# Optimization experiments

Measured on AMD Instinct MI355X. Metric: run time of the kernel, lower is better.

The kernel has to match this reference:

```python
import jax, jax.numpy as jnp
import numpy as np

N = 100000
E = 1600000
D_IN = 64
D_H = 64
D_OUT = 10
EPS_BN = 1e-5
EPS_NORM = 1e-12


def setup_inputs() -> dict:
    key = jax.random.key(0)
    ks = jax.random.split(key, 16)
    x = jax.random.normal(ks[0], (N, D_IN), dtype=jnp.float32)
    edge_index = jax.random.randint(ks[1], (2, E), 0, N, dtype=jnp.int64)
    def lin(k, fo, fi):
        s = 1.0 / np.sqrt(fi)
        return jax.random.uniform(k, (fo, fi), jnp.float32, -s, s)
    return {
        "x": x, "edge_index": edge_index,
        "Wl1": lin(ks[2], D_H, D_IN), "Wr1": lin(ks[3], D_H, D_IN), "b1": jnp.zeros((D_H,), jnp.float32),
        "g1": jnp.ones((D_H,), jnp.float32), "be1": jnp.zeros((D_H,), jnp.float32),
        "Wl2": lin(ks[4], D_H, D_H), "Wr2": lin(ks[5], D_H, D_H), "b2": jnp.zeros((D_H,), jnp.float32),
        "g2": jnp.ones((D_H,), jnp.float32), "be2": jnp.zeros((D_H,), jnp.float32),
        "Wl3": lin(ks[6], D_OUT, D_H), "Wr3": lin(ks[7], D_OUT, D_H), "b3": jnp.zeros((D_OUT,), jnp.float32),
    }


def _sage_conv(x, src, dst, Wl, Wr, b, normalize):
    # mean aggregation over incoming edges (messages flow src -> dst)
    agg = jax.ops.segment_sum(x[src], dst, num_segments=N)
    cnt = jax.ops.segment_sum(jnp.ones((src.shape[0],), x.dtype), dst, num_segments=N)
    mean = agg / jnp.clip(cnt, 1.0)[:, None]
    out = mean @ Wl.T + x @ Wr.T + b
    if normalize:
        nrm = jnp.sqrt(jnp.sum(out * out, axis=-1, keepdims=True))
        out = out / jnp.maximum(nrm, EPS_NORM)
    return out


def _batchnorm(x, gamma, beta):
    mu = jnp.mean(x, axis=0)
    var = jnp.mean((x - mu) ** 2, axis=0)  # biased var (training mode)
    return (x - mu) * jax.lax.rsqrt(var + EPS_BN) * gamma + beta


def reference(x, edge_index, Wl1, Wr1, b1, g1, be1, Wl2, Wr2, b2, g2, be2, Wl3, Wr3, b3):
    src, dst = edge_index[0], edge_index[1]
    h = _sage_conv(x, src, dst, Wl1, Wr1, b1, True)
    h = jax.nn.relu(_batchnorm(h, g1, be1))
    h = _sage_conv(h, src, dst, Wl2, Wr2, b2, True)
    h = jax.nn.relu(_batchnorm(h, g2, be2))
    h = _sage_conv(h, src, dst, Wl3, Wr3, b3, False)
    return h
```

## Files before the change

### kernel.cpp

```cpp
#include <hip/hip_runtime.h>
#include <hip/hip_bf16.h>

#define NN 100000
#define EE 1600000
#define BSZ 512
#define NBKT 196
#define CHUNK 8192
#define NCH 196

typedef short bf16x8 __attribute__((ext_vector_type(8)));
typedef float f32x4 __attribute__((ext_vector_type(4)));

__device__ inline unsigned short bf16_of(float f) {
    __hip_bfloat16 h = __float2bfloat16(f);
    return *reinterpret_cast<unsigned short*>(&h);
}
__device__ inline unsigned pack2(float a, float b) {
    return (unsigned)bf16_of(a) | ((unsigned)bf16_of(b) << 16);
}
__device__ inline float bflo(unsigned u) { return __uint_as_float(u << 16); }
__device__ inline float bfhi(unsigned u) { return __uint_as_float(u & 0xffff0000u); }


__global__ __launch_bounds__(256)
void k_ccount(const int* __restrict__ ei, int* __restrict__ ccount) {
    __shared__ int hist[NBKT];
    int tid = threadIdx.x;
    int e0 = blockIdx.x * CHUNK;
    int e1 = e0 + CHUNK; if (e1 > EE) e1 = EE;
    for (int i = tid; i < NBKT; i += 256) hist[i] = 0;
    __syncthreads();
    for (int e = e0 + tid; e < e1; e += 256)
        atomicAdd(&hist[ei[EE + e] >> 9], 1);
    __syncthreads();
    for (int i = tid; i < NBKT; i += 256)
        if (hist[i]) atomicAdd(&ccount[i], hist[i]);
}

__global__ void k_cscan(const int* __restrict__ ccount, int* __restrict__ cbase,
                        int* __restrict__ gcur) {
    __shared__ int s[256];
    int tid = threadIdx.x;
    int v = (tid < NBKT) ? ccount[tid] : 0;
    s[tid] = v;
    __syncthreads();
    for (int off = 1; off < 256; off <<= 1) {
        int t = (tid >= off) ? s[tid - off] : 0;
        __syncthreads();
        if (tid >= off) s[tid] += t;
        __syncthreads();
    }
    if (tid < NBKT) {
        int excl = s[tid] - v;
        cbase[tid] = excl;
        gcur[tid] = excl;
    }
    if (tid == NBKT - 1) cbase[NBKT] = s[tid];
}

__global__ __launch_bounds__(256)
void k_coarse(const int* __restrict__ ei, int* __restrict__ gcur, int* __restrict__ pairs) {
    __shared__ int hist[NBKT];
    __shared__ int base[NBKT];
    __shared__ int curs[NBKT];
    int tid = threadIdx.x;
    int e0 = blockIdx.x * CHUNK;
    int e1 = e0 + CHUNK; if (e1 > EE) e1 = EE;
    for (int i = tid; i < NBKT; i += 256) hist[i] = 0;
    __syncthreads();
    for (int e = e0 + tid; e < e1; e += 256)
        atomicAdd(&hist[ei[EE + e] >> 9], 1);
    __syncthreads();
    for (int i = tid; i < NBKT; i += 256) {
        base[i] = atomicAdd(&gcur[i], hist[i]);
        curs[i] = 0;
    }
    __syncthreads();
    for (int e = e0 + tid; e < e1; e += 256) {
        int src = ei[e];
        int dst = ei[EE + e];
        int b = dst >> 9;
        int off = atomicAdd(&curs[b], 1);
        pairs[base[b] + off] = (src << 9) | (dst & 511);
    }
}

__global__ __launch_bounds__(512)
void k_fine(const int* __restrict__ cbase, const int* __restrict__ pairs,
            int* __restrict__ rs, int* __restrict__ esrc) {
    __shared__ int deg[BSZ];
    __shared__ int s[BSZ];
    int b = blockIdx.x;
    int n0 = b * BSZ;
    int nlocal = NN - n0; if (nlocal > BSZ) nlocal = BSZ;
    int tid = threadIdx.x;
    deg[tid] = 0;
    __syncthreads();
    int e0 = cbase[b], e1 = cbase[b + 1];
    for (int e = e0 + tid; e < e1; e += 512)
        atomicAdd(&deg[pairs[e] & 511], 1);
    __syncthreads();
    int v = deg[tid];
    s[tid] = v;
    __syncthreads();
    for (int off = 1; off < 512; off <<= 1) {
        int t = (tid >= off) ? s[tid - off] : 0;
        __syncthreads();
        if (tid >= off) s[tid] += t;
        __syncthreads();
    }
    int excl = s[tid] - v;
    if (tid < nlocal) rs[n0 + tid] = e0 + excl;
    if (b == NBKT - 1 && tid == 0) rs[NN] = EE;
    deg[tid] = e0 + excl;
    __syncthreads();
    for (int e = e0 + tid; e < e1; e += 512) {
        int pk = pairs[e];
        int pos = atomicAdd(&deg[pk & 511], 1);
        esrc[pos] = pk >> 9;
    }
}

__global__ void k_tobf(const float4* __restrict__ src, ushort4* __restrict__ dst) {
    int i = blockIdx.x * 256 + threadIdx.x;
    if (i >= NN * 16) return;
    float4 v = src[i];
    dst[i] = make_ushort4(bf16_of(v.x), bf16_of(v.y), bf16_of(v.z), bf16_of(v.w));
}

__global__ void k_packW(const float* __restrict__ Wl1, const float* __restrict__ Wr1,
                        const float* __restrict__ Wl2, const float* __restrict__ Wr2,
                        unsigned short* __restrict__ w1, unsigned short* __restrict__ w2) {
    int tid = threadIdx.x;
    for (int i = tid; i < 8192; i += 256) {
        int n = i >> 7, k = i & 127;
        float v1 = (k < 64) ? Wl1[n * 64 + k] : Wr1[n * 64 + (k - 64)];
        w1[i] = bf16_of(v1);
        float v2 = (k < 64) ? Wl2[n * 64 + k] : Wr2[n * 64 + (k - 64)];
        w2[i] = bf16_of(v2);
    }
}

__global__ __launch_bounds__(256, 8)
void k_aggbf(const unsigned short* __restrict__ xbf, const int* __restrict__ rs,
             const int* __restrict__ esrc, unsigned short* __restrict__ meanbf,
             const float* __restrict__ sc, const float* __restrict__ sh) {
    int gid = blockIdx.x * 256 + threadIdx.x;
    int node = gid >> 6;
    if (node >= NN) return;
    int lane = threadIdx.x & 63;
    int c = lane & 7;
    int slot = lane >> 3;
    int s0 = rs[node], s1 = rs[node + 1];
    const uint4* xb = (const uint4*)xbf;
    float a0 = 0.f, a1 = 0.f, a2 = 0.f, a3 = 0.f, a4 = 0.f, a5 = 0.f, a6 = 0.f, a7 = 0.f;
    if (sc) {
        float4 scl = ((const float4*)sc)[2 * c], sch = ((const float4*)sc)[2 * c + 1];
        float4 shl = ((const float4*)sh)[2 * c], shh = ((const float4*)sh)[2 * c + 1];
        int p = s0 + slot;
        for (; p + 8 < s1; p += 16) {
            uint4 va = xb[esrc[p] * 8 + c];
            uint4 vb = xb[esrc[p + 8] * 8 + c];
            a0 += fmaxf(fmaf(bflo(va.x), scl.x, shl.x), 0.f);
            a1 += fmaxf(fmaf(bfhi(va.x), scl.y, shl.y), 0.f);
            a2 += fmaxf(fmaf(bflo(va.y), scl.z, shl.z), 0.f);
            a3 += fmaxf(fmaf(bfhi(va.y), scl.w, shl.w), 0.f);
            a4 += fmaxf(fmaf(bflo(va.z), sch.x, shh.x), 0.f);
            a5 += fmaxf(fmaf(bfhi(va.z), sch.y, shh.y), 0.f);
            a6 += fmaxf(fmaf(bflo(va.w), sch.z, shh.z), 0.f);
            a7 += fmaxf(fmaf(bfhi(va.w), sch.w, shh.w), 0.f);
            a0 += fmaxf(fmaf(bflo(vb.x), scl.x, shl.x), 0.f);
            a1 += fmaxf(fmaf(bfhi(vb.x), scl.y, shl.y), 0.f);
            a2 += fmaxf(fmaf(bflo(vb.y), scl.z, shl.z), 0.f);
            a3 += fmaxf(fmaf(bfhi(vb.y), scl.w, shl.w), 0.f);
            a4 += fmaxf(fmaf(bflo(vb.z), sch.x, shh.x), 0.f);
            a5 += fmaxf(fmaf(bfhi(vb.z), sch.y, shh.y), 0.f);
            a6 += fmaxf(fmaf(bflo(vb.w), sch.z, shh.z), 0.f);
            a7 += fmaxf(fmaf(bfhi(vb.w), sch.w, shh.w), 0.f);
        }
        if (p < s1) {
            uint4 va = xb[esrc[p] * 8 + c];
            a0 += fmaxf(fmaf(bflo(va.x), scl.x, shl.x), 0.f);
            a1 += fmaxf(fmaf(bfhi(va.x), scl.y, shl.y), 0.f);
            a2 += fmaxf(fmaf(bflo(va.y), scl.z, shl.z), 0.f);
            a3 += fmaxf(fmaf(bfhi(va.y), scl.w, shl.w), 0.f);
            a4 += fmaxf(fmaf(bflo(va.z), sch.x, shh.x), 0.f);
            a5 += fmaxf(fmaf(bfhi(va.z), sch.y, shh.y), 0.f);
            a6 += fmaxf(fmaf(bflo(va.w), sch.z, shh.z), 0.f);
            a7 += fmaxf(fmaf(bfhi(va.w), sch.w, shh.w), 0.f);
        }
    } else {
        int p = s0 + slot;
        for (; p + 8 < s1; p += 16) {
            uint4 va = xb[esrc[p] * 8 + c];
            uint4 vb = xb[esrc[p + 8] * 8 + c];
            a0 += bflo(va.x) + bflo(vb.x); a1 += bfhi(va.x) + bfhi(vb.x);
            a2 += bflo(va.y) + bflo(vb.y); a3 += bfhi(va.y) + bfhi(vb.y);
            a4 += bflo(va.z) + bflo(vb.z); a5 += bfhi(va.z) + bfhi(vb.z);
            a6 += bflo(va.w) + bflo(vb.w); a7 += bfhi(va.w) + bfhi(vb.w);
        }
        if (p < s1) {
            uint4 va = xb[esrc[p] * 8 + c];
            a0 += bflo(va.x); a1 += bfhi(va.x);
            a2 += bflo(va.y); a3 += bfhi(va.y);
            a4 += bflo(va.z); a5 += bfhi(va.z);
            a6 += bflo(va.w); a7 += bfhi(va.w);
        }
    }
#pragma unroll
    for (int m = 8; m <= 32; m <<= 1) {
        a0 += __shfl_xor(a0, m, 64); a1 += __shfl_xor(a1, m, 64);
        a2 += __shfl_xor(a2, m, 64); a3 += __shfl_xor(a3, m, 64);
        a4 += __shfl_xor(a4, m, 64); a5 += __shfl_xor(a5, m, 64);
        a6 += __shfl_xor(a6, m, 64); a7 += __shfl_xor(a7, m, 64);
    }
    if (slot == 0) {
        int cnt = s1 - s0; if (cnt < 1) cnt = 1;
        float inv = 1.0f / (float)cnt;
        uint4 o;
        o.x = pack2(a0 * inv, a1 * inv);
        o.y = pack2(a2 * inv, a3 * inv);
        o.z = pack2(a4 * inv, a5 * inv);
        o.w = pack2(a6 * inv, a7 * inv);
        ((uint4*)meanbf)[node * 8 + c] = o;
    }
}

__global__ __launch_bounds__(256, 4)
void k_sagemfma(const unsigned short* __restrict__ meanbf,
                const unsigned short* __restrict__ a2bf,
                const unsigned short* __restrict__ Wbf,
                const float* __restrict__ bias,
                unsigned short* __restrict__ outbf,
                float* __restrict__ partials,
                const float* __restrict__ sc, const float* __restrict__ sh) {
    __shared__ float sblk[64];
    __shared__ float qblk[64];
    const int tid = threadIdx.x;
    const int base = blockIdx.x * 64;
    const int col = tid & 15;
    const int q   = (tid >> 4) & 3;
    const int w   = tid >> 6;

    if (tid < 64) { sblk[tid] = 0.f; qblk[tid] = 0.f; }

    int gn = base + w * 16 + col; if (gn > NN - 1) gn = NN - 1;
    const uint4* mb = (const uint4*)meanbf;
    const uint4* ab = (const uint4*)a2bf;
    const uint4* wb = (const uint4*)Wbf;

    uint4 fa0 = mb[gn * 8 + q];
    uint4 fa1 = mb[gn * 8 + 4 + q];
    uint4 fa2 = ab[gn * 8 + q];
    uint4 fa3 = ab[gn * 8 + 4 + q];
    if (sc) {
        float4 s0 = ((const float4*)sc)[q * 2],     s1 = ((const float4*)sc)[q * 2 + 1];
        float4 h0 = ((const float4*)sh)[q * 2],     h1 = ((const float4*)sh)[q * 2 + 1];
        float4 s2 = ((const float4*)sc)[8 + q * 2], s3 = ((const float4*)sc)[8 + q * 2 + 1];
        float4 h2 = ((const float4*)sh)[8 + q * 2], h3 = ((const float4*)sh)[8 + q * 2 + 1];
        fa2.x = pack2(fmaxf(fmaf(bflo(fa2.x), s0.x, h0.x), 0.f),
                      fmaxf(fmaf(bfhi(fa2.x), s0.y, h0.y), 0.f));
        fa2.y = pack2(fmaxf(fmaf(bflo(fa2.y), s0.z, h0.z), 0.f),
                      fmaxf(fmaf(bfhi(fa2.y), s0.w, h0.w), 0.f));
        fa2.z = pack2(fmaxf(fmaf(bflo(fa2.z), s1.x, h1.x), 0.f),
                      fmaxf(fmaf(bfhi(fa2.z), s1.y, h1.y), 0.f));
        fa2.w = pack2(fmaxf(fmaf(bflo(fa2.w), s1.z, h1.z), 0.f),
                      fmaxf(fmaf(bfhi(fa2.w), s1.w, h1.w), 0.f));
        fa3.x = pack2(fmaxf(fmaf(bflo(fa3.x), s2.x, h2.x), 0.f),
                      fmaxf(fmaf(bfhi(fa3.x), s2.y, h2.y), 0.f));
        fa3.y = pack2(fmaxf(fmaf(bflo(fa3.y), s2.z, h2.z), 0.f),
                      fmaxf(fmaf(bfhi(fa3.y), s2.w, h2.w), 0.f));
        fa3.z = pack2(fmaxf(fmaf(bflo(fa3.z), s3.x, h3.x), 0.f),
                      fmaxf(fmaf(bfhi(fa3.z), s3.y, h3.y), 0.f));
        fa3.w = pack2(fmaxf(fmaf(bflo(fa3.w), s3.z, h3.z), 0.f),
                      fmaxf(fmaf(bfhi(fa3.w), s3.w, h3.w), 0.f));
    }
    uint4 fa[4] = {fa0, fa1, fa2, fa3};

    f32x4 acc0 = {0.f, 0.f, 0.f, 0.f}, acc1 = acc0, acc2 = acc0, acc3 = acc0;
#pragma unroll
    for (int c = 0; c < 4; ++c) {
        uint4 b0 = wb[(0 * 16 + col) * 16 + c * 4 + q];
        uint4 b1 = wb[(1 * 16 + col) * 16 + c * 4 + q];
        uint4 b2 = wb[(2 * 16 + col) * 16 + c * 4 + q];
        uint4 b3 = wb[(3 * 16 + col) * 16 + c * 4 + q];
        bf16x8 a = *(const bf16x8*)&fa[c];
        acc0 = __builtin_amdgcn_mfma_f32_16x16x32_bf16(a, *(const bf16x8*)&b0, acc0, 0, 0, 0);
        acc1 = __builtin_amdgcn_mfma_f32_16x16x32_bf16(a, *(const bf16x8*)&b1, acc1, 0, 0, 0);
        acc2 = __builtin_amdgcn_mfma_f32_16x16x32_bf16(a, *(const bf16x8*)&b2, acc2, 0, 0, 0);
        acc3 = __builtin_amdgcn_mfma_f32_16x16x32_bf16(a, *(const bf16x8*)&b3, acc3, 0, 0, 0);
    }

    float bb0 = bias[col], bb1 = bias[16 + col], bb2 = bias[32 + col], bb3 = bias[48 + col];
    float sj0 = 0.f, sj1 = 0.f, sj2 = 0.f, sj3 = 0.f;
    float qj0 = 0.f, qj1 = 0.f, qj2 = 0.f, qj3 = 0.f;
#pragma unroll
    for (int r = 0; r < 4; ++r) {
        int go = base + w * 16 + q * 4 + r;
        float o0 = acc0[r] + bb0, o1 = acc1[r] + bb1;
        float o2 = acc2[r] + bb2, o3 = acc3[r] + bb3;
        float ssv = o0 * o0 + o1 * o1 + o2 * o2 + o3 * o3;
        ssv += __shfl_xor(ssv, 1, 64);
        ssv += __shfl_xor(ssv, 2, 64);
        ssv += __shfl_xor(ssv, 4, 64);
        ssv += __shfl_xor(ssv, 8, 64);
        float inv = 1.0f / fmaxf(sqrtf(ssv), 1e-12f);
        o0 *= inv; o1 *= inv; o2 *= inv; o3 *= inv;
        if (go < NN) {
            outbf[go * 64 + col]      = bf16_of(o0);
            outbf[go * 64 + 16 + col] = bf16_of(o1);
            outbf[go * 64 + 32 + col] = bf16_of(o2);
            outbf[go * 64 + 48 + col] = bf16_of(o3);
            sj0 += o0; sj1 += o1; sj2 += o2; sj3 += o3;
            qj0 += o0 * o0; qj1 += o1 * o1; qj2 += o2 * o2; qj3 += o3 * o3;
        }
    }
#pragma unroll
    for (int m = 16; m <= 32; m <<= 1) {
        sj0 += __shfl_xor(sj0, m, 64); sj1 += __shfl_xor(sj1, m, 64);
        sj2 += __shfl_xor(sj2, m, 64); sj3 += __shfl_xor(sj3, m, 64);
        qj0 += __shfl_xor(qj0, m, 64); qj1 += __shfl_xor(qj1, m, 64);
        qj2 += __shfl_xor(qj2, m, 64); qj3 += __shfl_xor(qj3, m, 64);
    }
    __syncthreads();
    if (q == 0) {
        atomicAdd(&sblk[col], sj0);      atomicAdd(&qblk[col], qj0);
        atomicAdd(&sblk[16 + col], sj1); atomicAdd(&qblk[16 + col], qj1);
        atomicAdd(&sblk[32 + col], sj2); atomicAdd(&qblk[32 + col], qj2);
        atomicAdd(&sblk[48 + col], sj3); atomicAdd(&qblk[48 + col], qj3);
    }
    __syncthreads();
    if (tid < 128)
        partials[blockIdx.x * 128 + tid] = (tid < 64) ? sblk[tid] : qblk[tid - 64];
}

__global__ __launch_bounds__(256)
void k_bnred(const float* __restrict__ partials, int nblk, float* __restrict__ red) {
    __shared__ float s[256];
    int tid = threadIdx.x;
    int idx = tid & 127, half = tid >> 7;
    float a0 = 0.f, a1 = 0.f, a2 = 0.f, a3 = 0.f;
    int r = blockIdx.x * 2 + half;
    for (; r + 192 < nblk; r += 256) {
        a0 += partials[r * 128 + idx];
        a1 += partials[(r + 64) * 128 + idx];
        a2 += partials[(r + 128) * 128 + idx];
        a3 += partials[(r + 192) * 128 + idx];
    }
    for (; r < nblk; r += 64) a0 += partials[r * 128 + idx];
    s[tid] = (a0 + a1) + (a2 + a3);
    __syncthreads();
    if (tid < 128) red[blockIdx.x * 128 + tid] = s[tid] + s[tid + 128];
}

__global__ void k_bnfin(const float* __restrict__ red,
                        const float* __restrict__ g, const float* __restrict__ be,
                        float* __restrict__ scale, float* __restrict__ shift) {
    __shared__ float s[256];
    int tid = threadIdx.x;
    int idx = tid & 127, half = tid >> 7;
    float a = 0.f;
#pragma unroll
    for (int r = half; r < 32; r += 2)
        a += red[r * 128 + idx];
    s[tid] = a;
    __syncthreads();
    if (tid < 128) s[tid] += s[tid + 128];
    __syncthreads();
    if (tid < 64) {
        float mu = s[tid] / (float)NN;
        float var = s[64 + tid] / (float)NN - mu * mu;
        var = fmaxf(var, 0.0f);
        float sc = g[tid] / sqrtf(var + 1e-5f);
        scale[tid] = sc;
        shift[tid] = be[tid] - mu * sc;
    }
}

__global__ __launch_bounds__(256)
void k_project(const unsigned short* __restrict__ h,
               const float* __restrict__ sc, const float* __restrict__ sh,
               const float* __restrict__ Wl, const float* __restrict__ Wr,
               const float* __restrict__ bias,
               float* __restrict__ zl, float* __restrict__ zr) {
    __shared__ float Alds[64 * 128];
    __shared__ float Wlds[64 * 32];
    const int tid = threadIdx.x;
    const int base = blockIdx.x * 128;

#pragma unroll
    for (int i = 0; i < 8; ++i) {
        int idx = i * 256 + tid;
        int f = idx & 31, k = idx >> 5;
        float v = 0.0f;
        if (f < 16) { if (f < 10) v = Wl[f * 64 + k]; }
        else        { if (f - 16 < 10) v = Wr[(f - 16) * 64 + k]; }
        Wlds[k * 32 + f] = v;
    }
    {
        const uint4* h4 = (const uint4*)h;
        const float4* sc4p = (const float4*)sc;
        const float4* sh4p = (const float4*)sh;
#pragma unroll
        for (int i = 0; i < 4; ++i) {
            int idx = i * 256 + tid;
            int node = idx & 127, cb = idx >> 7;
            int gn = base + node; if (gn > NN - 1) gn = NN - 1;
            uint4 u = h4[gn * 8 + cb];
            float4 sA = sc4p[cb * 2], sB = sc4p[cb * 2 + 1];
            float4 hA = sh4p[cb * 2], hB = sh4p[cb * 2 + 1];
            int k0 = cb * 8;
            Alds[(k0 + 0) * 128 + node] = fmaxf(fmaf(bflo(u.x), sA.x, hA.x), 0.f);
            Alds[(k0 + 1) * 128 + node] = fmaxf(fmaf(bfhi(u.x), sA.y, hA.y), 0.f);
            Alds[(k0 + 2) * 128 + node] = fmaxf(fmaf(bflo(u.y), sA.z, hA.z), 0.f);
            Alds[(k0 + 3) * 128 + node] = fmaxf(fmaf(bfhi(u.y), sA.w, hA.w), 0.f);
            Alds[(k0 + 4) * 128 + node] = fmaxf(fmaf(bflo(u.z), sB.x, hB.x), 0.f);
            Alds[(k0 + 5) * 128 + node] = fmaxf(fmaf(bfhi(u.z), sB.y, hB.y), 0.f);
            Alds[(k0 + 6) * 128 + node] = fmaxf(fmaf(bflo(u.w), sB.z, hB.z), 0.f);
            Alds[(k0 + 7) * 128 + node] = fmaxf(fmaf(bfhi(u.w), sB.w, hB.w), 0.f);
        }
    }
    __syncthreads();

    const int fg = tid & 7;
    const int ng = tid >> 3;

    float acc[4][4] = {};
#pragma unroll 4
    for (int k = 0; k < 64; ++k) {
        const float4 a = *(const float4*)(Alds + k * 128 + (ng << 2));
        const float4 w = *(const float4*)(Wlds + k * 32 + (fg << 2));
        const float av[4] = {a.x, a.y, a.z, a.w};
        const float wv[4] = {w.x, w.y, w.z, w.w};
#pragma unroll
        for (int i = 0; i < 4; ++i)
#pragma unroll
            for (int j = 0; j < 4; ++j)
                acc[i][j] = fmaf(av[i], wv[j], acc[i][j]);
    }

    if (fg == 3 || fg == 7) return;
    float4* dst = (fg < 4) ? (float4*)zl : (float4*)zr;
    int fq = (fg < 4) ? fg : fg - 4;
    float bx = 0.f, by = 0.f, bz = 0.f, bw = 0.f;
    if (fg >= 4) {
        int f0 = fq * 4;
        bx = (f0 + 0 < 10) ? bias[f0 + 0] : 0.f;
        by = (f0 + 1 < 10) ? bias[f0 + 1] : 0.f;
        bz = (f0 + 2 < 10) ? bias[f0 + 2] : 0.f;
        bw = (f0 + 3 < 10) ? bias[f0 + 3] : 0.f;
    }
#pragma unroll
    for (int i = 0; i < 4; ++i) {
        int gn = base + (ng << 2) + i;
        if (gn < NN)
            dst[gn * 3 + fq] = make_float4(acc[i][0] + bx, acc[i][1] + by,
                                           acc[i][2] + bz, acc[i][3] + bw);
    }
}

__global__ __launch_bounds__(256)
void k_agg10(const int* __restrict__ rs, const int* __restrict__ esrc,
             const float* __restrict__ zl, const float* __restrict__ zr,
             float* __restrict__ out) {
    int gid = blockIdx.x * 256 + threadIdx.x;
    unsigned node = (unsigned)gid / 3u;
    int j = gid - (int)node * 3;
    if (node >= NN) return;
    int s0 = rs[node], s1 = rs[node + 1];
    const float4* zl4 = (const float4*)zl;
    float4 acc = make_float4(0.f, 0.f, 0.f, 0.f);
    int p = s0;
    for (; p + 3 < s1; p += 4) {
        float4 v0 = zl4[esrc[p] * 3 + j];
        float4 v1 = zl4[esrc[p + 1] * 3 + j];
        float4 v2 = zl4[esrc[p + 2] * 3 + j];
        float4 v3 = zl4[esrc[p + 3] * 3 + j];
        acc.x += (v0.x + v1.x) + (v2.x + v3.x);
        acc.y += (v0.y + v1.y) + (v2.y + v3.y);
        acc.z += (v0.z + v1.z) + (v2.z + v3.z);
        acc.w += (v0.w + v1.w) + (v2.w + v3.w);
    }
    for (; p < s1; ++p) {
        float4 v = zl4[esrc[p] * 3 + j];
        acc.x += v.x; acc.y += v.y; acc.z += v.z; acc.w += v.w;
    }
    int cnt = s1 - s0; if (cnt < 1) cnt = 1;
    float inv = 1.0f / (float)cnt;
    float4 r = ((const float4*)zr)[node * 3 + j];
    r.x = fmaf(acc.x, inv, r.x); r.y = fmaf(acc.y, inv, r.y);
    r.z = fmaf(acc.z, inv, r.z); r.w = fmaf(acc.w, inv, r.w);
    float2* o2 = (float2*)(out + (size_t)node * 10);
    if (j < 2) {
        o2[j * 2 + 0] = make_float2(r.x, r.y);
        o2[j * 2 + 1] = make_float2(r.z, r.w);
    } else {
        o2[4] = make_float2(r.x, r.y);
    }
}


extern "C" void kernel_launch(void* const* d_in, const int* in_sizes, int n_in,
                              void* d_out, int out_size, void* d_ws, size_t ws_size,
                              hipStream_t stream) {
    const float* x   = (const float*)d_in[0];
    const int*   ei  = (const int*)d_in[1];
    const float* Wl1 = (const float*)d_in[2];
    const float* Wr1 = (const float*)d_in[3];
    const float* b1  = (const float*)d_in[4];
    const float* g1  = (const float*)d_in[5];
    const float* be1 = (const float*)d_in[6];
    const float* Wl2 = (const float*)d_in[7];
    const float* Wr2 = (const float*)d_in[8];
    const float* b2  = (const float*)d_in[9];
    const float* g2  = (const float*)d_in[10];
    const float* be2 = (const float*)d_in[11];
    const float* Wl3 = (const float*)d_in[12];
    const float* Wr3 = (const float*)d_in[13];
    const float* b3  = (const float*)d_in[14];
    float* out = (float*)d_out;

    char* w = (char*)d_ws;
    auto alloc = [&](size_t bytes) -> void* {
        void* p = (void*)w;
        w += (bytes + 255) & ~(size_t)255;
        return p;
    };
    int*   ccount = (int*)alloc(256 * 4);
    int*   cbase  = (int*)alloc(256 * 4);
    int*   gcur   = (int*)alloc(256 * 4);
    int*   rs     = (int*)alloc((size_t)(NN + 1) * 4);
    int*   esrc   = (int*)alloc((size_t)EE * 4);
    float* scratch= (float*)alloc((size_t)NN * 64 * 4);
    unsigned short* xbf    = (unsigned short*)alloc((size_t)NN * 64 * 2);
    unsigned short* h1bf   = (unsigned short*)alloc((size_t)NN * 64 * 2);
    unsigned short* meanbf = (unsigned short*)alloc((size_t)NN * 64 * 2);
    unsigned short* wbf1   = (unsigned short*)alloc(8192 * 2);
    unsigned short* wbf2   = (unsigned short*)alloc(8192 * 2);
    float* partials = (float*)alloc((size_t)1563 * 128 * 4);
    float* red    = (float*)alloc(32 * 128 * 4);
    float* scsh   = (float*)alloc(256 * 4);
    int*   pairs  = (int*)scratch;
    float* zl     = scratch;
    float* zr     = scratch + (size_t)NN * 12;

    hipMemsetAsync(ccount, 0, 256 * 4, stream);

    k_ccount<<<NCH, 256, 0, stream>>>(ei, ccount);
    k_cscan<<<1, 256, 0, stream>>>(ccount, cbase, gcur);
    k_coarse<<<NCH, 256, 0, stream>>>(ei, gcur, pairs);
    k_fine<<<NBKT, 512, 0, stream>>>(cbase, pairs, rs, esrc);
    k_tobf<<<(NN * 16 + 255) / 256, 256, 0, stream>>>((const float4*)x, (ushort4*)xbf);
    k_packW<<<1, 256, 0, stream>>>(Wl1, Wr1, Wl2, Wr2, wbf1, wbf2);

    const int aggBlocks  = (NN * 64) / 256;
    const int sageBlocks = (NN + 63) / 64;
    const int projBlocks = (NN + 127) / 128;
    const int a10Blocks  = (NN * 3 + 255) / 256;

    k_aggbf<<<aggBlocks, 256, 0, stream>>>(xbf, rs, esrc, meanbf, nullptr, nullptr);
    k_sagemfma<<<sageBlocks, 256, 0, stream>>>(meanbf, xbf, wbf1, b1, h1bf,
                                               partials, nullptr, nullptr);
    k_bnred<<<32, 256, 0, stream>>>(partials, sageBlocks, red);
    k_bnfin<<<1, 256, 0, stream>>>(red, g1, be1, scsh + 0, scsh + 64);

    k_aggbf<<<aggBlocks, 256, 0, stream>>>(h1bf, rs, esrc, meanbf, scsh + 0, scsh + 64);
    k_sagemfma<<<sageBlocks, 256, 0, stream>>>(meanbf, h1bf, wbf2, b2, xbf,
                                               partials, scsh + 0, scsh + 64);
    k_bnred<<<32, 256, 0, stream>>>(partials, sageBlocks, red);
    k_bnfin<<<1, 256, 0, stream>>>(red, g2, be2, scsh + 128, scsh + 192);

    k_project<<<projBlocks, 256, 0, stream>>>(xbf, scsh + 128, scsh + 192,
                                              Wl3, Wr3, b3, zl, zr);
    k_agg10<<<a10Blocks, 256, 0, stream>>>(rs, esrc, zl, zr, out);
}
```

Baseline: 339.9 us.

## Fuse BN reduction into SAGE kernel via last-block finalize and merge prep kernels

```diff
diff --git a/kernel.cpp b/kernel.cpp
--- a/kernel.cpp
+++ b/kernel.cpp
@@ -121,23 +121,32 @@
     }
 }
 
-__global__ void k_tobf(const float4* __restrict__ src, ushort4* __restrict__ dst) {
-    int i = blockIdx.x * 256 + threadIdx.x;
-    if (i >= NN * 16) return;
-    float4 v = src[i];
-    dst[i] = make_ushort4(bf16_of(v.x), bf16_of(v.y), bf16_of(v.z), bf16_of(v.w));
-}
-
-__global__ void k_packW(const float* __restrict__ Wl1, const float* __restrict__ Wr1,
-                        const float* __restrict__ Wl2, const float* __restrict__ Wr2,
-                        unsigned short* __restrict__ w1, unsigned short* __restrict__ w2) {
-    int tid = threadIdx.x;
-    for (int i = tid; i < 8192; i += 256) {
-        int n = i >> 7, k = i & 127;
-        float v1 = (k < 64) ? Wl1[n * 64 + k] : Wr1[n * 64 + (k - 64)];
-        w1[i] = bf16_of(v1);
-        float v2 = (k < 64) ? Wl2[n * 64 + k] : Wr2[n * 64 + (k - 64)];
-        w2[i] = bf16_of(v2);
+__global__ __launch_bounds__(256)
+void k_tobfW(const float4* __restrict__ src, ushort4* __restrict__ dst,
+             const float* __restrict__ Wl1, const float* __restrict__ Wr1,
+             const float* __restrict__ Wl2, const float* __restrict__ Wr2,
+             unsigned short* __restrict__ w1, unsigned short* __restrict__ w2,
+             int* __restrict__ ccount, float* __restrict__ p64a,
+             float* __restrict__ p64b, int* __restrict__ counters) {
+    int b = blockIdx.x, tid = threadIdx.x;
+    if (b < 6250) {
+        int i = b * 256 + tid;
+        if (i < NN * 16) {
+            float4 v = src[i];
+            dst[i] = make_ushort4(bf16_of(v.x), bf16_of(v.y), bf16_of(v.z), bf16_of(v.w));
+        }
+    } else {
+        for (int i = tid; i < 8192; i += 256) {
+            int n = i >> 7, k = i & 127;
+            float v1 = (k < 64) ? Wl1[n * 64 + k] : Wr1[n * 64 + (k - 64)];
+            w1[i] = bf16_of(v1);
+            float v2 = (k < 64) ? Wl2[n * 64 + k] : Wr2[n * 64 + (k - 64)];
+            w2[i] = bf16_of(v2);
+            p64a[i] = 0.f;
+            p64b[i] = 0.f;
+        }
+        if (tid < NBKT) ccount[tid] = 0;
+        if (tid < 2) counters[tid] = 0;
     }
 }
 
@@ -232,10 +241,16 @@
                 const unsigned short* __restrict__ Wbf,
                 const float* __restrict__ bias,
                 unsigned short* __restrict__ outbf,
-                float* __restrict__ partials,
+                float* __restrict__ p64,
+                int* __restrict__ counter,
+                const float* __restrict__ g, const float* __restrict__ be,
+                float* __restrict__ scale, float* __restrict__ shift,
                 const float* __restrict__ sc, const float* __restrict__ sh) {
     __shared__ float sblk[64];
     __shared__ float qblk[64];
+    __shared__ float red2[256];
+    __shared__ float fin[128];
+    __shared__ int lastflag;
     const int tid = threadIdx.x;
     const int base = blockIdx.x * 64;
     const int col = tid & 15;
@@ -331,49 +346,33 @@
     }
     __syncthreads();
     if (tid < 128)
-        partials[blockIdx.x * 128 + tid] = (tid < 64) ? sblk[tid] : qblk[tid - 64];
-}
-
-__global__ __launch_bounds__(256)
-void k_bnred(const float* __restrict__ partials, int nblk, float* __restrict__ red) {
-    __shared__ float s[256];
-    int tid = threadIdx.x;
-    int idx = tid & 127, half = tid >> 7;
-    float a0 = 0.f, a1 = 0.f, a2 = 0.f, a3 = 0.f;
-    int r = blockIdx.x * 2 + half;
-    for (; r + 192 < nblk; r += 256) {
-        a0 += partials[r * 128 + idx];
-        a1 += partials[(r + 64) * 128 + idx];
-        a2 += partials[(r + 128) * 128 + idx];
-        a3 += partials[(r + 192) * 128 + idx];
-    }
-    for (; r < nblk; r += 64) a0 += partials[r * 128 + idx];
-    s[tid] = (a0 + a1) + (a2 + a3);
-    __syncthreads();
-    if (tid < 128) red[blockIdx.x * 128 + tid] = s[tid] + s[tid + 128];
-}
-
-__global__ void k_bnfin(const float* __restrict__ red,
-                        const float* __restrict__ g, const float* __restrict__ be,
-                        float* __restrict__ scale, float* __restrict__ shift) {
-    __shared__ float s[256];
-    int tid = threadIdx.x;
-    int idx = tid & 127, half = tid >> 7;
-    float a = 0.f;
-#pragma unroll
-    for (int r = half; r < 32; r += 2)
-        a += red[r * 128 + idx];
-    s[tid] = a;
-    __syncthreads();
-    if (tid < 128) s[tid] += s[tid + 128];
-    __syncthreads();
-    if (tid < 64) {
-        float mu = s[tid] / (float)NN;
-        float var = s[64 + tid] / (float)NN - mu * mu;
-        var = fmaxf(var, 0.0f);
-        float sc = g[tid] / sqrtf(var + 1e-5f);
-        scale[tid] = sc;
-        shift[tid] = be[tid] - mu * sc;
+        atomicAdd(&p64[(blockIdx.x & 63) * 128 + tid],
+                  (tid < 64) ? sblk[tid] : qblk[tid - 64]);
+    __threadfence();
+    __syncthreads();
+    if (tid == 0) {
+        int old = atomicAdd(counter, 1);
+        lastflag = (old == (int)gridDim.x - 1) ? 1 : 0;
+    }
+    __syncthreads();
+    if (lastflag) {
+        __threadfence();
+        int idx = tid & 127, half = tid >> 7;
+        float a = 0.f;
+#pragma unroll
+        for (int r = half; r < 64; r += 2)
+            a += p64[r * 128 + idx];
+        red2[tid] = a;
+        __syncthreads();
+        if (tid < 128) fin[tid] = red2[tid] + red2[tid + 128];
+        __syncthreads();
+        if (tid < 64) {
+            float mu = fin[tid] / (float)NN;
+            float var = fmaxf(fin[64 + tid] / (float)NN - mu * mu, 0.f);
+            float scv = g[tid] / sqrtf(var + 1e-5f);
+            scale[tid] = scv;
+            shift[tid] = be[tid] - mu * scv;
+        }
     }
 }
 
@@ -529,6 +528,7 @@
     int*   ccount = (int*)alloc(256 * 4);
     int*   cbase  = (int*)alloc(256 * 4);
     int*   gcur   = (int*)alloc(256 * 4);
+    int*   counters = (int*)alloc(256 * 4);
     int*   rs     = (int*)alloc((size_t)(NN + 1) * 4);
     int*   esrc   = (int*)alloc((size_t)EE * 4);
     float* scratch= (float*)alloc((size_t)NN * 64 * 4);
@@ -537,21 +537,20 @@
     unsigned short* meanbf = (unsigned short*)alloc((size_t)NN * 64 * 2);
     unsigned short* wbf1   = (unsigned short*)alloc(8192 * 2);
     unsigned short* wbf2   = (unsigned short*)alloc(8192 * 2);
-    float* partials = (float*)alloc((size_t)1563 * 128 * 4);
-    float* red    = (float*)alloc(32 * 128 * 4);
+    float* p64a   = (float*)alloc(8192 * 4);
+    float* p64b   = (float*)alloc(8192 * 4);
     float* scsh   = (float*)alloc(256 * 4);
     int*   pairs  = (int*)scratch;
     float* zl     = scratch;
     float* zr     = scratch + (size_t)NN * 12;
 
-    hipMemsetAsync(ccount, 0, 256 * 4, stream);
-
+    k_tobfW<<<6251, 256, 0, stream>>>((const float4*)x, (ushort4*)xbf,
+                                      Wl1, Wr1, Wl2, Wr2, wbf1, wbf2,
+                                      ccount, p64a, p64b, counters);
     k_ccount<<<NCH, 256, 0, stream>>>(ei, ccount);
     k_cscan<<<1, 256, 0, stream>>>(ccount, cbase, gcur);
     k_coarse<<<NCH, 256, 0, stream>>>(ei, gcur, pairs);
     k_fine<<<NBKT, 512, 0, stream>>>(cbase, pairs, rs, esrc);
-    k_tobf<<<(NN * 16 + 255) / 256, 256, 0, stream>>>((const float4*)x, (ushort4*)xbf);
-    k_packW<<<1, 256, 0, stream>>>(Wl1, Wr1, Wl2, Wr2, wbf1, wbf2);
 
     const int aggBlocks  = (NN * 64) / 256;
     const int sageBlocks = (NN + 63) / 64;
@@ -560,15 +559,13 @@
 
     k_aggbf<<<aggBlocks, 256, 0, stream>>>(xbf, rs, esrc, meanbf, nullptr, nullptr);
     k_sagemfma<<<sageBlocks, 256, 0, stream>>>(meanbf, xbf, wbf1, b1, h1bf,
-                                               partials, nullptr, nullptr);
-    k_bnred<<<32, 256, 0, stream>>>(partials, sageBlocks, red);
-    k_bnfin<<<1, 256, 0, stream>>>(red, g1, be1, scsh + 0, scsh + 64);
+                                               p64a, counters + 0, g1, be1,
+                                               scsh + 0, scsh + 64, nullptr, nullptr);
 
     k_aggbf<<<aggBlocks, 256, 0, stream>>>(h1bf, rs, esrc, meanbf, scsh + 0, scsh + 64);
     k_sagemfma<<<sageBlocks, 256, 0, stream>>>(meanbf, h1bf, wbf2, b2, xbf,
-                                               partials, scsh + 0, scsh + 64);
-    k_bnred<<<32, 256, 0, stream>>>(partials, sageBlocks, red);
-    k_bnfin<<<1, 256, 0, stream>>>(red, g2, be2, scsh + 128, scsh + 192);
+                                               p64b, counters + 1, g2, be2,
+                                               scsh + 128, scsh + 192, scsh + 0, scsh + 64);
 
     k_project<<<projBlocks, 256, 0, stream>>>(xbf, scsh + 128, scsh + 192,
                                               Wl3, Wr3, b3, zl, zr);
```

Measured after the change: 655.9 us. 93.0% more time.
